# Kernel optimization log

Measured on AMD Instinct MI355X. Metric: run time of the kernel, lower is better.

The kernel has to match this reference:

```python
import jax, jax.numpy as jnp
import numpy as np

N = 50000        # links * batches
E = 1000000      # edges per frame
T = 10           # frame_num
H = 8            # graph_embedding_size


def setup_inputs() -> dict:
    key = jax.random.key(0)
    ks = jax.random.split(key, 20)
    w = lambda k, s: (jax.random.normal(k, s, jnp.float32) * 0.1)
    return {
        "x": jax.random.normal(ks[0], (N, T, 2), jnp.float32),
        "edge_index": jax.random.randint(ks[1], (2, T, E), 0, N),
        "edge_attr": jax.random.uniform(ks[2], (E, T, 1), jnp.float32),
        # mlp1: [1+H, 32, 32] + Lin(32,1)+Sigmoid
        "m1_w1": w(ks[3], (1 + H, 32)), "m1_b1": jnp.zeros((32,), jnp.float32),
        "m1_w2": w(ks[4], (32, 32)),     "m1_b2": jnp.zeros((32,), jnp.float32),
        "m1_w3": w(ks[5], (32, 1)),      "m1_b3": jnp.zeros((1,), jnp.float32),
        # mlp2: [1+1+H, 32, H]
        "m2_w1": w(ks[6], (2 + H, 32)),  "m2_b1": jnp.zeros((32,), jnp.float32),
        "m2_w2": w(ks[7], (32, H)),      "m2_b2": jnp.zeros((H,), jnp.float32),
        # h2o: [H, 16] + Lin(16,1)+Sigmoid
        "o_w1": w(ks[8], (H, 16)),       "o_b1": jnp.zeros((16,), jnp.float32),
        "o_w2": w(ks[9], (16, 1)),       "o_b2": jnp.zeros((1,), jnp.float32),
    }


def reference(x, edge_index, edge_attr,
              m1_w1, m1_b1, m1_w2, m1_b2, m1_w3, m1_b3,
              m2_w1, m2_b1, m2_w2, m2_b2,
              o_w1, o_b1, o_w2, o_b2):
    n_nodes = x.shape[0]
    hid = m2_b2.shape[0]
    AGG_MEAN, AGG_VAR = 0.0, 1.0  # undefined globals in source; identity norm

    def step(hidden, inputs):
        x_t, ei_t, ea_t = inputs                 # [N,2], [2,E], [E,1]
        xh = jnp.concatenate([x_t, hidden], 1)   # [N, 2+H]
        src, dst = ei_t[0], ei_t[1]              # PyG: x_j = x[src], agg at dst
        xj = xh[src]                             # [E, 2+H] gather
        feat = jnp.concatenate([xj[:, :1], xj[:, 2:]], 1)  # [E, 1+H]
        h = jax.nn.relu(feat @ m1_w1 + m1_b1)
        h = jax.nn.relu(h @ m1_w2 + m1_b2)
        msg = jax.nn.sigmoid(h @ m1_w3 + m1_b3) * ea_t      # [E,1]
        agg = jax.ops.segment_sum(msg, dst, num_segments=n_nodes)  # [N,1]
        norm = (agg - AGG_MEAN) / AGG_VAR
        upd_in = jnp.concatenate([xh[:, 1:], norm], 1)      # [N, 2+H]
        u = jax.nn.relu(upd_in @ m2_w1 + m2_b1)
        u = jax.nn.relu(u @ m2_w2 + m2_b2)
        hidden_new = jnp.tanh(u)                            # [N,H]
        o = jax.nn.relu(hidden_new @ o_w1 + o_b1)
        out = jax.nn.sigmoid(o @ o_w2 + o_b2)               # [N,1]
        return hidden_new, out

    x_seq = jnp.transpose(x, (1, 0, 2))            # [T,N,2]
    ei_seq = jnp.transpose(edge_index, (1, 0, 2))  # [T,2,E]
    ea_seq = jnp.transpose(edge_attr, (1, 0, 2))   # [T,E,1]
    h0 = jnp.zeros((n_nodes, hid), x.dtype)
    _, outs = jax.lax.scan(step, h0, (x_seq, ei_seq, ea_seq))
    return outs  # [T, N, 1]
```

## Files before the change

kernel.cpp:

```cpp
#include <hip/hip_runtime.h>

#define NN 50000
#define TT 10
#define EE 1000000

#define NB 391
#define BN 128
#define NBP 512
#define CAP 3072
#define CHUNK 2048
#define NCHUNK 489
#define KPT (CHUNK / 256)
#define SPILLCAP 8192

__device__ __forceinline__ float sigmoidf_(float v) { return 1.0f / (1.0f + __expf(-v)); }
__device__ __forceinline__ float reluf_(float v) { return v > 0.0f ? v : 0.0f; }

__device__ __forceinline__ float4 ld4_(const float* __restrict__ p) {
    return *reinterpret_cast<const float4*>(p);
}
__device__ __forceinline__ void fma_row8(float* acc, const float* __restrict__ w, float f) {
    float4 a = ld4_(w), b = ld4_(w + 4);
    acc[0] += f * a.x; acc[1] += f * a.y; acc[2] += f * a.z; acc[3] += f * a.w;
    acc[4] += f * b.x; acc[5] += f * b.y; acc[6] += f * b.z; acc[7] += f * b.w;
}

__device__ __forceinline__ float mlp1_eval_g(const float* feat,
                                             const float* __restrict__ w1,
                                             const float* __restrict__ b1,
                                             const float* __restrict__ w2,
                                             const float* __restrict__ b2,
                                             const float* __restrict__ w3,
                                             const float* __restrict__ b3) {
    float h1[32];
#pragma unroll
    for (int j = 0; j < 32; ++j) h1[j] = b1[j];
#pragma unroll
    for (int i = 0; i < 9; ++i) {
        float f = feat[i];
#pragma unroll
        for (int j = 0; j < 32; ++j) h1[j] += f * w1[i * 32 + j];
    }
#pragma unroll
    for (int j = 0; j < 32; ++j) h1[j] = reluf_(h1[j]);
    float h2[32];
#pragma unroll
    for (int j = 0; j < 32; ++j) h2[j] = b2[j];
#pragma unroll
    for (int i = 0; i < 32; ++i) {
        float f = h1[i];
#pragma unroll
        for (int j = 0; j < 32; ++j) h2[j] += f * w2[i * 32 + j];
    }
    float acc = b3[0];
#pragma unroll
    for (int j = 0; j < 32; ++j) acc += reluf_(h2[j]) * w3[j];
    return sigmoidf_(acc);
}

__global__ void pre_kernel(const float* __restrict__ x,
                           const float* __restrict__ w1, const float* __restrict__ b1,
                           const float* __restrict__ w2, const float* __restrict__ b2,
                           const float* __restrict__ w3, const float* __restrict__ b3,
                           float* __restrict__ hidden, float* __restrict__ msg_base,
                           float* __restrict__ agg,
                           float* __restrict__ x0T, float* __restrict__ x1T,
                           unsigned* __restrict__ gcnt, unsigned* __restrict__ spillCnt,
                           int sorted) {
    int g = blockIdx.x * blockDim.x + threadIdx.x;
    if (g < NB * TT) gcnt[g] = 0u;
    if (g == 0) spillCnt[0] = 0u;
    if (g >= NN) return;
    float x00;
    if (sorted) {
        const float2* xr = reinterpret_cast<const float2*>(x + (size_t)g * TT * 2);
        float x0v[TT], x1v[TT];
#pragma unroll
        for (int tt = 0; tt < TT; ++tt) { float2 p = xr[tt]; x0v[tt] = p.x; x1v[tt] = p.y; }
#pragma unroll
        for (int tt = 0; tt < TT; ++tt) { x0T[tt * NN + g] = x0v[tt]; x1T[tt * NN + g] = x1v[tt]; }
        x00 = x0v[0];
    } else {
        x00 = x[(size_t)g * TT * 2];
    }
    agg[g] = 0.0f;
    float feat[9];
    feat[0] = x00;
#pragma unroll
    for (int k = 0; k < 8; ++k) feat[1 + k] = 0.0f;
    msg_base[g] = mlp1_eval_g(feat, w1, b1, w2, b2, w3, b3);
#pragma unroll
    for (int k = 0; k < 8; ++k) hidden[g * 8 + k] = 0.0f;
}

__global__ __launch_bounds__(256) void reorder_kernel(const int* __restrict__ ei,
                                                      const float* __restrict__ ea,
                                                      unsigned* __restrict__ gcnt,
                                                      int4* __restrict__ regions,
                                                      int4* __restrict__ spill,
                                                      unsigned* __restrict__ spillCnt) {
    __shared__ int4 stg[CHUNK];
    __shared__ unsigned h4[4][NBP];
    __shared__ unsigned lbase[NBP], cur[NBP], gbase[NBP];
    __shared__ unsigned bscan[256];
    __shared__ unsigned cnt_s;
    const int t = blockIdx.x, c = blockIdx.y;
    const int tid = threadIdx.x, w = tid >> 6;

    for (int i = tid; i < 4 * NBP; i += 256) (&h4[0][0])[i] = 0u;
    __syncthreads();

    const int* srcp = ei + (size_t)t * EE;
    const int* dstp = ei + (size_t)(TT + t) * EE;
    int se[KPT], de[KPT];
    float ev[KPT];
#pragma unroll
    for (int k = 0; k < KPT; ++k) {
        int e = c * CHUNK + k * 256 + tid;
        if (e < EE) {
            se[k] = srcp[e];
            de[k] = dstp[e];
            ev[k] = ea[(size_t)e * TT + t];
            atomicAdd(&h4[w][(unsigned)de[k] >> 7], 1u);
        } else {
            de[k] = -1; se[k] = 0; ev[k] = 0.0f;
        }
    }
    __syncthreads();

    unsigned c0 = h4[0][2 * tid] + h4[1][2 * tid] + h4[2][2 * tid] + h4[3][2 * tid];
    unsigned c1 = h4[0][2 * tid + 1] + h4[1][2 * tid + 1] + h4[2][2 * tid + 1] + h4[3][2 * tid + 1];
    unsigned mys = c0 + c1;
    bscan[tid] = mys;
    __syncthreads();
    for (int off = 1; off < 256; off <<= 1) {
        unsigned vv = (tid >= off) ? bscan[tid - off] : 0u;
        __syncthreads();
        bscan[tid] += vv;
        __syncthreads();
    }
    unsigned excl = bscan[tid] - mys;
    lbase[2 * tid] = excl;           cur[2 * tid] = excl;
    lbase[2 * tid + 1] = excl + c0;  cur[2 * tid + 1] = excl + c0;
    if (tid == 255) cnt_s = bscan[255];
    {
        int b0 = 2 * tid, b1 = 2 * tid + 1;
        gbase[b0] = (b0 < NB) ? atomicAdd(&gcnt[t * NB + b0], c0) : 0u;
        gbase[b1] = (b1 < NB) ? atomicAdd(&gcnt[t * NB + b1], c1) : 0u;
    }
    __syncthreads();

#pragma unroll
    for (int k = 0; k < KPT; ++k) {
        if (de[k] >= 0) {
            unsigned b = (unsigned)de[k] >> 7;
            unsigned slot = atomicAdd(&cur[b], 1u);
            stg[slot] = make_int4(se[k], de[k], __float_as_int(ev[k]), 0);
        }
    }
    __syncthreads();

    const unsigned cnt = cnt_s;
    for (unsigned i = tid; i < cnt; i += 256) {
        int4 rec = stg[i];
        unsigned b = (unsigned)rec.y >> 7;
        unsigned g = gbase[b] + (i - lbase[b]);
        if (g < CAP) {
            regions[((size_t)(t * NB + b)) * CAP + g] = rec;
        } else {
            unsigned sp = atomicAdd(spillCnt, 1u);
            if (sp < SPILLCAP) spill[sp] = make_int4(rec.x, rec.y, rec.z, t);
        }
    }
}

__global__ __launch_bounds__(512) void edge_node_kernel(
        const float* __restrict__ x0T, const float* __restrict__ x1T,
        const int4* __restrict__ regions, const unsigned* __restrict__ gcnt,
        const int4* __restrict__ spill, const unsigned* __restrict__ spillCnt,
        const float* __restrict__ m1w1, const float* __restrict__ m1b1,
        const float* __restrict__ m1w2, const float* __restrict__ m1b2,
        const float* __restrict__ m1w3, const float* __restrict__ m1b3,
        const float* __restrict__ m2w1, const float* __restrict__ m2b1,
        const float* __restrict__ m2w2, const float* __restrict__ m2b2,
        const float* __restrict__ ow1, const float* __restrict__ ob1,
        const float* __restrict__ ow2, const float* __restrict__ ob2,
        float* __restrict__ hidden, float* __restrict__ msg_base,
        float* __restrict__ out, int t) {
    __shared__ float acc_s[BN];
    const int b = blockIdx.x, tid = threadIdx.x;
    if (tid < BN) acc_s[tid] = 0.0f;
    __syncthreads();

    {
        unsigned cnt = gcnt[t * NB + b];
        if (cnt > CAP) cnt = CAP;
        const int4* p = regions + ((size_t)(t * NB + b)) * CAP;
        for (unsigned i = tid; i < cnt; i += 512) {
            int4 rec = p[i];
            atomicAdd(&acc_s[rec.y & (BN - 1)], msg_base[rec.x] * __int_as_float(rec.z));
        }
        unsigned sp = spillCnt[0];
        for (unsigned j = tid; j < sp; j += 512) {
            int4 rec = spill[j];
            if (rec.w == t && ((unsigned)rec.y >> 7) == (unsigned)b)
                atomicAdd(&acc_s[rec.y & (BN - 1)], msg_base[rec.x] * __int_as_float(rec.z));
        }
    }
    __syncthreads();

    const int n = b * BN + (tid >> 2);
    const int q = tid & 3;
    if (n >= NN) return;

    const float a = acc_s[tid >> 2];
    const float x1 = x1T[t * NN + n];

    float2 hme = *reinterpret_cast<const float2*>(hidden + (size_t)n * 8 + q * 2);
    float hid[8];
    hid[0] = hme.x; hid[1] = hme.y;
    hid[2] = __shfl_xor(hid[0], 1); hid[3] = __shfl_xor(hid[1], 1);
    hid[4] = __shfl_xor(hid[0], 2); hid[5] = __shfl_xor(hid[1], 2);
    hid[6] = __shfl_xor(hid[2], 2); hid[7] = __shfl_xor(hid[3], 2);

    float acc[8];
    {
        float4 bA = ld4_(m2b1 + q * 8), bB = ld4_(m2b1 + q * 8 + 4);
        acc[0] = bA.x; acc[1] = bA.y; acc[2] = bA.z; acc[3] = bA.w;
        acc[4] = bB.x; acc[5] = bB.y; acc[6] = bB.z; acc[7] = bB.w;
    }
    fma_row8(acc, m2w1 + q * 8, x1);
#pragma unroll
    for (int g = 0; g < 4; ++g) {
        int rq = (q ^ g) * 2;
        fma_row8(acc, m2w1 + (size_t)(1 + rq) * 32 + q * 8, hid[g * 2 + 0]);
        fma_row8(acc, m2w1 + (size_t)(2 + rq) * 32 + q * 8, hid[g * 2 + 1]);
    }
    fma_row8(acc, m2w1 + (size_t)9 * 32 + q * 8, a);
    float u1[8];
#pragma unroll
    for (int jj = 0; jj < 8; ++jj) u1[jj] = reluf_(acc[jj]);

    float pk[8];
#pragma unroll
    for (int k = 0; k < 8; ++k) pk[k] = 0.0f;
#pragma unroll
    for (int jj = 0; jj < 8; ++jj)
        fma_row8(pk, m2w2 + (size_t)(q * 8 + jj) * 8, u1[jj]);
#pragma unroll
    for (int k = 0; k < 8; ++k) {
        pk[k] += __shfl_xor(pk[k], 1);
        pk[k] += __shfl_xor(pk[k], 2);
    }
    float hn[8];
    {
        float4 b2A = ld4_(m2b2), b2B = ld4_(m2b2 + 4);
        hn[0] = tanhf(reluf_(pk[0] + b2A.x));
        hn[1] = tanhf(reluf_(pk[1] + b2A.y));
        hn[2] = tanhf(reluf_(pk[2] + b2A.z));
        hn[3] = tanhf(reluf_(pk[3] + b2A.w));
        hn[4] = tanhf(reluf_(pk[4] + b2B.x));
        hn[5] = tanhf(reluf_(pk[5] + b2B.y));
        hn[6] = tanhf(reluf_(pk[6] + b2B.z));
        hn[7] = tanhf(reluf_(pk[7] + b2B.w));
    }
    if (q == 0) {
        *reinterpret_cast<float4*>(hidden + (size_t)n * 8)     = make_float4(hn[0], hn[1], hn[2], hn[3]);
        *reinterpret_cast<float4*>(hidden + (size_t)n * 8 + 4) = make_float4(hn[4], hn[5], hn[6], hn[7]);
    }

    float o1v[4];
    {
        float4 ob = ld4_(ob1 + q * 4);
        o1v[0] = ob.x; o1v[1] = ob.y; o1v[2] = ob.z; o1v[3] = ob.w;
    }
#pragma unroll
    for (int k = 0; k < 8; ++k) {
        float4 wv = ld4_(ow1 + k * 16 + q * 4);
        o1v[0] += hn[k] * wv.x; o1v[1] += hn[k] * wv.y;
        o1v[2] += hn[k] * wv.z; o1v[3] += hn[k] * wv.w;
    }
    {
        float4 w2v = ld4_(ow2 + q * 4);
        float oop = reluf_(o1v[0]) * w2v.x + reluf_(o1v[1]) * w2v.y +
                    reluf_(o1v[2]) * w2v.z + reluf_(o1v[3]) * w2v.w;
        oop += __shfl_xor(oop, 1);
        oop += __shfl_xor(oop, 2);
        if (q == 0) out[t * NN + n] = sigmoidf_(oop + ob2[0]);
    }

    if (t < TT - 1) {
        float feat0 = x0T[(t + 1) * NN + n];
        float h1[8];
        {
            float4 bA = ld4_(m1b1 + q * 8), bB = ld4_(m1b1 + q * 8 + 4);
            h1[0] = bA.x; h1[1] = bA.y; h1[2] = bA.z; h1[3] = bA.w;
            h1[4] = bB.x; h1[5] = bB.y; h1[6] = bB.z; h1[7] = bB.w;
        }
        fma_row8(h1, m1w1 + q * 8, feat0);
#pragma unroll
        for (int k = 0; k < 8; ++k)
            fma_row8(h1, m1w1 + (size_t)(1 + k) * 32 + q * 8, hn[k]);
#pragma unroll
        for (int jj = 0; jj < 8; ++jj) h1[jj] = reluf_(h1[jj]);

        float h1x[32];
#pragma unroll
        for (int jj = 0; jj < 8; ++jj) h1x[jj] = h1[jj];
#pragma unroll
        for (int jj = 0; jj < 8; ++jj) h1x[8 + jj]  = __shfl_xor(h1x[jj], 1);
#pragma unroll
        for (int jj = 0; jj < 8; ++jj) h1x[16 + jj] = __shfl_xor(h1x[jj], 2);
#pragma unroll
        for (int jj = 0; jj < 8; ++jj) h1x[24 + jj] = __shfl_xor(h1x[8 + jj], 2);

        float acc8[8];
        {
            float4 bA = ld4_(m1b2 + q * 8), bB = ld4_(m1b2 + q * 8 + 4);
            acc8[0] = bA.x; acc8[1] = bA.y; acc8[2] = bA.z; acc8[3] = bA.w;
            acc8[4] = bB.x; acc8[5] = bB.y; acc8[6] = bB.z; acc8[7] = bB.w;
        }
#pragma unroll
        for (int g = 0; g < 4; ++g) {
            int rb = (q ^ g) * 8;
#pragma unroll
            for (int jj = 0; jj < 8; ++jj)
                fma_row8(acc8, m1w2 + (size_t)(rb + jj) * 32 + q * 8, h1x[g * 8 + jj]);
        }
        float s3;
        {
            float4 w3a = ld4_(m1w3 + q * 8), w3b = ld4_(m1w3 + q * 8 + 4);
            s3 = reluf_(acc8[0]) * w3a.x + reluf_(acc8[1]) * w3a.y +
                 reluf_(acc8[2]) * w3a.z + reluf_(acc8[3]) * w3a.w +
                 reluf_(acc8[4]) * w3b.x + reluf_(acc8[5]) * w3b.y +
                 reluf_(acc8[6]) * w3b.z + reluf_(acc8[7]) * w3b.w;
        }
        s3 += __shfl_xor(s3, 1);
        s3 += __shfl_xor(s3, 2);
        if (q == 0) msg_base[n] = sigmoidf_(s3 + m1b3[0]);
    }
}

__global__ void edge_kernel(const int* __restrict__ ei, const float* __restrict__ ea,
                            const float* __restrict__ msg_base, float* __restrict__ agg,
                            int t) {
    int g = blockIdx.x * blockDim.x + threadIdx.x;
    int e0 = g * 2;
    if (e0 >= EE) return;
    const int2 s = *reinterpret_cast<const int2*>(ei + (size_t)t * EE + e0);
    const int2 d = *reinterpret_cast<const int2*>(ei + (size_t)(TT + t) * EE + e0);
    atomicAdd(&agg[d.x], msg_base[s.x] * ea[(size_t)e0 * TT + t]);
    atomicAdd(&agg[d.y], msg_base[s.y] * ea[(size_t)(e0 + 1) * TT + t]);
}

__global__ __launch_bounds__(256) void node4_legacy_kernel(
        const float* __restrict__ x,
        const float* __restrict__ m1w1, const float* __restrict__ m1b1,
        const float* __restrict__ m1w2, const float* __restrict__ m1b2,
        const float* __restrict__ m1w3, const float* __restrict__ m1b3,
        const float* __restrict__ m2w1, const float* __restrict__ m2b1,
        const float* __restrict__ m2w2, const float* __restrict__ m2b2,
        const float* __restrict__ ow1, const float* __restrict__ ob1,
        const float* __restrict__ ow2, const float* __restrict__ ob2,
        float* __restrict__ hidden, float* __restrict__ msg_base,
        float* __restrict__ agg, float* __restrict__ out, int t) {
    const int gid = blockIdx.x * 256 + threadIdx.x;
    const int n = gid >> 2;
    const int q = gid & 3;
    if (n >= NN) return;
    const float a = agg[n];
    const float x1 = x[(size_t)n * TT * 2 + t * 2 + 1];
    float2 hme = *reinterpret_cast<const float2*>(hidden + (size_t)n * 8 + q * 2);
    float hid[8];
    hid[0] = hme.x; hid[1] = hme.y;
    hid[2] = __shfl_xor(hid[0], 1); hid[3] = __shfl_xor(hid[1], 1);
    hid[4] = __shfl_xor(hid[0], 2); hid[5] = __shfl_xor(hid[1], 2);
    hid[6] = __shfl_xor(hid[2], 2); hid[7] = __shfl_xor(hid[3], 2);
    float acc[8];
    {
        float4 bA = ld4_(m2b1 + q * 8), bB = ld4_(m2b1 + q * 8 + 4);
        acc[0] = bA.x; acc[1] = bA.y; acc[2] = bA.z; acc[3] = bA.w;
        acc[4] = bB.x; acc[5] = bB.y; acc[6] = bB.z; acc[7] = bB.w;
    }
    fma_row8(acc, m2w1 + q * 8, x1);
#pragma unroll
    for (int g = 0; g < 4; ++g) {
        int rq = (q ^ g) * 2;
        fma_row8(acc, m2w1 + (size_t)(1 + rq) * 32 + q * 8, hid[g * 2 + 0]);
        fma_row8(acc, m2w1 + (size_t)(2 + rq) * 32 + q * 8, hid[g * 2 + 1]);
    }
    fma_row8(acc, m2w1 + (size_t)9 * 32 + q * 8, a);
    float u1[8];
#pragma unroll
    for (int jj = 0; jj < 8; ++jj) u1[jj] = reluf_(acc[jj]);
    float pk[8];
#pragma unroll
    for (int k = 0; k < 8; ++k) pk[k] = 0.0f;
#pragma unroll
    for (int jj = 0; jj < 8; ++jj)
        fma_row8(pk, m2w2 + (size_t)(q * 8 + jj) * 8, u1[jj]);
#pragma unroll
    for (int k = 0; k < 8; ++k) {
        pk[k] += __shfl_xor(pk[k], 1);
        pk[k] += __shfl_xor(pk[k], 2);
    }
    float hn[8];
    {
        float4 b2A = ld4_(m2b2), b2B = ld4_(m2b2 + 4);
        hn[0] = tanhf(reluf_(pk[0] + b2A.x));
        hn[1] = tanhf(reluf_(pk[1] + b2A.y));
        hn[2] = tanhf(reluf_(pk[2] + b2A.z));
        hn[3] = tanhf(reluf_(pk[3] + b2A.w));
        hn[4] = tanhf(reluf_(pk[4] + b2B.x));
        hn[5] = tanhf(reluf_(pk[5] + b2B.y));
        hn[6] = tanhf(reluf_(pk[6] + b2B.z));
        hn[7] = tanhf(reluf_(pk[7] + b2B.w));
    }
    if (q == 0) {
        *reinterpret_cast<float4*>(hidden + (size_t)n * 8)     = make_float4(hn[0], hn[1], hn[2], hn[3]);
        *reinterpret_cast<float4*>(hidden + (size_t)n * 8 + 4) = make_float4(hn[4], hn[5], hn[6], hn[7]);
    }
    float o1v[4];
    {
        float4 ob = ld4_(ob1 + q * 4);
        o1v[0] = ob.x; o1v[1] = ob.y; o1v[2] = ob.z; o1v[3] = ob.w;
    }
#pragma unroll
    for (int k = 0; k < 8; ++k) {
        float4 wv = ld4_(ow1 + k * 16 + q * 4);
        o1v[0] += hn[k] * wv.x; o1v[1] += hn[k] * wv.y;
        o1v[2] += hn[k] * wv.z; o1v[3] += hn[k] * wv.w;
    }
    {
        float4 w2v = ld4_(ow2 + q * 4);
        float oop = reluf_(o1v[0]) * w2v.x + reluf_(o1v[1]) * w2v.y +
                    reluf_(o1v[2]) * w2v.z + reluf_(o1v[3]) * w2v.w;
        oop += __shfl_xor(oop, 1);
        oop += __shfl_xor(oop, 2);
        if (q == 0) out[t * NN + n] = sigmoidf_(oop + ob2[0]);
    }
    if (t < TT - 1) {
        float feat0 = x[(size_t)n * TT * 2 + (t + 1) * 2];
        float h1[8];
        {
            float4 bA = ld4_(m1b1 + q * 8), bB = ld4_(m1b1 + q * 8 + 4);
            h1[0] = bA.x; h1[1] = bA.y; h1[2] = bA.z; h1[3] = bA.w;
            h1[4] = bB.x; h1[5] = bB.y; h1[6] = bB.z; h1[7] = bB.w;
        }
        fma_row8(h1, m1w1 + q * 8, feat0);
#pragma unroll
        for (int k = 0; k < 8; ++k)
            fma_row8(h1, m1w1 + (size_t)(1 + k) * 32 + q * 8, hn[k]);
#pragma unroll
        for (int jj = 0; jj < 8; ++jj) h1[jj] = reluf_(h1[jj]);
        float h1x[32];
#pragma unroll
        for (int jj = 0; jj < 8; ++jj) h1x[jj] = h1[jj];
#pragma unroll
        for (int jj = 0; jj < 8; ++jj) h1x[8 + jj]  = __shfl_xor(h1x[jj], 1);
#pragma unroll
        for (int jj = 0; jj < 8; ++jj) h1x[16 + jj] = __shfl_xor(h1x[jj], 2);
#pragma unroll
        for (int jj = 0; jj < 8; ++jj) h1x[24 + jj] = __shfl_xor(h1x[8 + jj], 2);
        float acc8[8];
        {
            float4 bA = ld4_(m1b2 + q * 8), bB = ld4_(m1b2 + q * 8 + 4);
            acc8[0] = bA.x; acc8[1] = bA.y; acc8[2] = bA.z; acc8[3] = bA.w;
            acc8[4] = bB.x; acc8[5] = bB.y; acc8[6] = bB.z; acc8[7] = bB.w;
        }
#pragma unroll
        for (int g = 0; g < 4; ++g) {
            int rb = (q ^ g) * 8;
#pragma unroll
            for (int jj = 0; jj < 8; ++jj)
                fma_row8(acc8, m1w2 + (size_t)(rb + jj) * 32 + q * 8, h1x[g * 8 + jj]);
        }
        float s3;
        {
            float4 w3a = ld4_(m1w3 + q * 8), w3b = ld4_(m1w3 + q * 8 + 4);
            s3 = reluf_(acc8[0]) * w3a.x + reluf_(acc8[1]) * w3a.y +
                 reluf_(acc8[2]) * w3a.z + reluf_(acc8[3]) * w3a.w +
                 reluf_(acc8[4]) * w3b.x + reluf_(acc8[5]) * w3b.y +
                 reluf_(acc8[6]) * w3b.z + reluf_(acc8[7]) * w3b.w;
        }
        s3 += __shfl_xor(s3, 1);
        s3 += __shfl_xor(s3, 2);
        if (q == 0) {
            msg_base[n] = sigmoidf_(s3 + m1b3[0]);
            agg[n] = 0.0f;
        }
    }
}

extern "C" void kernel_launch(void* const* d_in, const int* in_sizes, int n_in,
                              void* d_out, int out_size, void* d_ws, size_t ws_size,
                              hipStream_t stream) {
    (void)in_sizes; (void)n_in; (void)out_size;
    const float* x    = (const float*)d_in[0];
    const int*   ei   = (const int*)d_in[1];
    const float* ea   = (const float*)d_in[2];
    const float* m1w1 = (const float*)d_in[3];
    const float* m1b1 = (const float*)d_in[4];
    const float* m1w2 = (const float*)d_in[5];
    const float* m1b2 = (const float*)d_in[6];
    const float* m1w3 = (const float*)d_in[7];
    const float* m1b3 = (const float*)d_in[8];
    const float* m2w1 = (const float*)d_in[9];
    const float* m2b1 = (const float*)d_in[10];
    const float* m2w2 = (const float*)d_in[11];
    const float* m2b2 = (const float*)d_in[12];
    const float* ow1  = (const float*)d_in[13];
    const float* ob1  = (const float*)d_in[14];
    const float* ow2  = (const float*)d_in[15];
    const float* ob2  = (const float*)d_in[16];
    float* out = (float*)d_out;

    char* wp = (char*)d_ws;
    float* hidden   = (float*)wp; wp += (size_t)NN * 8 * 4;
    float* msg_base = (float*)wp; wp += (size_t)NN * 4;
    float* agg      = (float*)wp; wp += (size_t)NN * 4;
    float* x0T      = (float*)wp; wp += (size_t)NN * TT * 4;
    float* x1T      = (float*)wp; wp += (size_t)NN * TT * 4;
    int4*  regions  = (int4*)wp;  wp += (size_t)NB * TT * CAP * 16;
    int4*  spill    = (int4*)wp;  wp += (size_t)SPILLCAP * 16;
    unsigned* gcnt    = (unsigned*)wp; wp += (size_t)NB * TT * 4;
    unsigned* spillCnt = (unsigned*)wp; wp += 64;
    size_t need = (size_t)(wp - (char*)d_ws);

    int sorted = (ws_size >= need) ? 1 : 0;

    dim3 blk(256);
    int nodeBlocks = (NN + 255) / 256;
    int edgeBlocksLegacy = (EE / 2 + 255) / 256;
    int node4BlocksLegacy = (NN * 4 + 255) / 256;

    pre_kernel<<<nodeBlocks, blk, 0, stream>>>(x, m1w1, m1b1, m1w2, m1b2, m1w3, m1b3,
                                               hidden, msg_base, agg, x0T, x1T,
                                               gcnt, spillCnt, sorted);
    if (sorted) {
        reorder_kernel<<<dim3(TT, NCHUNK), blk, 0, stream>>>(ei, ea, gcnt, regions,
                                                             spill, spillCnt);
        for (int t = 0; t < TT; ++t) {
            edge_node_kernel<<<NB, dim3(512), 0, stream>>>(
                x0T, x1T, regions, gcnt, spill, spillCnt,
                m1w1, m1b1, m1w2, m1b2, m1w3, m1b3,
                m2w1, m2b1, m2w2, m2b2,
                ow1, ob1, ow2, ob2,
                hidden, msg_base, out, t);
        }
    } else {
        for (int t = 0; t < TT; ++t) {
            edge_kernel<<<edgeBlocksLegacy, blk, 0, stream>>>(ei, ea, msg_base, agg, t);
            node4_legacy_kernel<<<node4BlocksLegacy, blk, 0, stream>>>(
                x, m1w1, m1b1, m1w2, m1b2, m1w3, m1b3,
                m2w1, m2b1, m2w2, m2b2,
                ow1, ob1, ow2, ob2,
                hidden, msg_base, agg, out, t);
        }
    }
}
```

Baseline: 593.9 us.

## Transpose edge attrs, pack region records, stage weights in LDS, double-buffer messages

The pre kernel now transposes edge_attr into a frame-major buffer so the reorder kernel reads it coalesced instead of with a stride of 10 floats. Region records shrink from int4 to int2 by packing the source index and the local destination into one word, which halves region write and read traffic. The edge_node kernel stages all MLP weights in shared memory rather than reading them from global memory. Message values are double-buffered (msgA/msgB) to fix a read/write race on msg_base across blocks. The cost is an extra 40MB transpose pass and a larger workspace requirement, which may make the sorted path fall back if the workspace is too small.

```diff
diff --git a/kernel.cpp b/kernel.cpp
--- a/kernel.cpp
+++ b/kernel.cpp
@@ -13,19 +13,36 @@
 #define KPT (CHUNK / 256)
 #define SPILLCAP 8192
 
+#define OFF_M2W1 0
+#define OFF_M2B1 320
+#define OFF_M2W2 352
+#define OFF_M2B2 608
+#define OFF_OW1  616
+#define OFF_OB1  744
+#define OFF_OW2  760
+#define OFF_M1W1 776
+#define OFF_M1B1 1064
+#define OFF_M1W2 1096
+#define OFF_M1B2 2120
+#define OFF_M1W3 2152
+#define OFF_OB2  2184
+#define OFF_M1B3 2185
+#define WTOT     2188
+
 __device__ __forceinline__ float sigmoidf_(float v) { return 1.0f / (1.0f + __expf(-v)); }
 __device__ __forceinline__ float reluf_(float v) { return v > 0.0f ? v : 0.0f; }
 
 __device__ __forceinline__ float4 ld4_(const float* __restrict__ p) {
     return *reinterpret_cast<const float4*>(p);
 }
-__device__ __forceinline__ void fma_row8(float* acc, const float* __restrict__ w, float f) {
-    float4 a = ld4_(w), b = ld4_(w + 4);
+__device__ __forceinline__ void fma_row8(float* acc, const float* w, float f) {
+    float4 a = *reinterpret_cast<const float4*>(w);
+    float4 b = *reinterpret_cast<const float4*>(w + 4);
     acc[0] += f * a.x; acc[1] += f * a.y; acc[2] += f * a.z; acc[3] += f * a.w;
     acc[4] += f * b.x; acc[5] += f * b.y; acc[6] += f * b.z; acc[7] += f * b.w;
 }
 
-__device__ __forceinline__ float mlp1_eval_g(const float* feat,
+__device__ __forceinline__ float mlp1_frame0(float x00,
                                              const float* __restrict__ w1,
                                              const float* __restrict__ b1,
                                              const float* __restrict__ w2,
@@ -34,15 +51,7 @@
                                              const float* __restrict__ b3) {
     float h1[32];
 #pragma unroll
-    for (int j = 0; j < 32; ++j) h1[j] = b1[j];
-#pragma unroll
-    for (int i = 0; i < 9; ++i) {
-        float f = feat[i];
-#pragma unroll
-        for (int j = 0; j < 32; ++j) h1[j] += f * w1[i * 32 + j];
-    }
-#pragma unroll
-    for (int j = 0; j < 32; ++j) h1[j] = reluf_(h1[j]);
+    for (int j = 0; j < 32; ++j) h1[j] = reluf_(b1[j] + x00 * w1[j]);
     float h2[32];
 #pragma unroll
     for (int j = 0; j < 32; ++j) h2[j] = b2[j];
@@ -59,17 +68,29 @@
 }
 
 __global__ void pre_kernel(const float* __restrict__ x,
+                           const float* __restrict__ ea,
                            const float* __restrict__ w1, const float* __restrict__ b1,
                            const float* __restrict__ w2, const float* __restrict__ b2,
                            const float* __restrict__ w3, const float* __restrict__ b3,
-                           float* __restrict__ hidden, float* __restrict__ msg_base,
+                           float* __restrict__ hidden, float* __restrict__ msgA,
                            float* __restrict__ agg,
                            float* __restrict__ x0T, float* __restrict__ x1T,
+                           float* __restrict__ eaT,
                            unsigned* __restrict__ gcnt, unsigned* __restrict__ spillCnt,
                            int sorted) {
     int g = blockIdx.x * blockDim.x + threadIdx.x;
-    if (g < NB * TT) gcnt[g] = 0u;
-    if (g == 0) spillCnt[0] = 0u;
+    if (sorted) {
+        if (g < EE) {
+            const float2* row = reinterpret_cast<const float2*>(ea + (size_t)g * TT);
+            float v[TT];
+#pragma unroll
+            for (int c = 0; c < 5; ++c) { float2 p = row[c]; v[2 * c] = p.x; v[2 * c + 1] = p.y; }
+#pragma unroll
+            for (int tt = 0; tt < TT; ++tt) eaT[(size_t)tt * EE + g] = v[tt];
+        }
+        if (g < NB * TT) gcnt[g] = 0u;
+        if (g == 0) spillCnt[0] = 0u;
+    }
     if (g >= NN) return;
     float x00;
     if (sorted) {
@@ -84,19 +105,15 @@
         x00 = x[(size_t)g * TT * 2];
     }
     agg[g] = 0.0f;
-    float feat[9];
-    feat[0] = x00;
-#pragma unroll
-    for (int k = 0; k < 8; ++k) feat[1 + k] = 0.0f;
-    msg_base[g] = mlp1_eval_g(feat, w1, b1, w2, b2, w3, b3);
+    msgA[g] = mlp1_frame0(x00, w1, b1, w2, b2, w3, b3);
 #pragma unroll
     for (int k = 0; k < 8; ++k) hidden[g * 8 + k] = 0.0f;
 }
 
 __global__ __launch_bounds__(256) void reorder_kernel(const int* __restrict__ ei,
-                                                      const float* __restrict__ ea,
+                                                      const float* __restrict__ eaT,
                                                       unsigned* __restrict__ gcnt,
-                                                      int4* __restrict__ regions,
+                                                      int2* __restrict__ regions,
                                                       int4* __restrict__ spill,
                                                       unsigned* __restrict__ spillCnt) {
     __shared__ int4 stg[CHUNK];
@@ -120,7 +137,7 @@
         if (e < EE) {
             se[k] = srcp[e];
             de[k] = dstp[e];
-            ev[k] = ea[(size_t)e * TT + t];
+            ev[k] = eaT[(size_t)t * EE + e];
             atomicAdd(&h4[w][(unsigned)de[k] >> 7], 1u);
         } else {
             de[k] = -1; se[k] = 0; ev[k] = 0.0f;
@@ -166,7 +183,8 @@
         unsigned b = (unsigned)rec.y >> 7;
         unsigned g = gbase[b] + (i - lbase[b]);
         if (g < CAP) {
-            regions[((size_t)(t * NB + b)) * CAP + g] = rec;
+            unsigned u = (unsigned)rec.x | (((unsigned)rec.y & 127u) << 17);
+            regions[((size_t)(t * NB + b)) * CAP + g] = make_int2((int)u, rec.z);
         } else {
             unsigned sp = atomicAdd(spillCnt, 1u);
             if (sp < SPILLCAP) spill[sp] = make_int4(rec.x, rec.y, rec.z, t);
@@ -176,7 +194,7 @@
 
 __global__ __launch_bounds__(512) void edge_node_kernel(
         const float* __restrict__ x0T, const float* __restrict__ x1T,
-        const int4* __restrict__ regions, const unsigned* __restrict__ gcnt,
+        const int2* __restrict__ regions, const unsigned* __restrict__ gcnt,
         const int4* __restrict__ spill, const unsigned* __restrict__ spillCnt,
         const float* __restrict__ m1w1, const float* __restrict__ m1b1,
         const float* __restrict__ m1w2, const float* __restrict__ m1b2,
@@ -185,26 +203,45 @@
         const float* __restrict__ m2w2, const float* __restrict__ m2b2,
         const float* __restrict__ ow1, const float* __restrict__ ob1,
         const float* __restrict__ ow2, const float* __restrict__ ob2,
-        float* __restrict__ hidden, float* __restrict__ msg_base,
-        float* __restrict__ out, int t) {
+        float* __restrict__ hidden, const float* __restrict__ msgIn,
+        float* __restrict__ msgOut, float* __restrict__ out, int t) {
+    __shared__ __align__(16) float wsh[WTOT];
     __shared__ float acc_s[BN];
     const int b = blockIdx.x, tid = threadIdx.x;
+
+    for (int i = tid; i < 320; i += 512) wsh[OFF_M2W1 + i] = m2w1[i];
+    for (int i = tid; i < 256; i += 512) wsh[OFF_M2W2 + i] = m2w2[i];
+    for (int i = tid; i < 288; i += 512) wsh[OFF_M1W1 + i] = m1w1[i];
+    for (int i = tid; i < 1024; i += 512) wsh[OFF_M1W2 + i] = m1w2[i];
+    if (tid < 32) {
+        wsh[OFF_M2B1 + tid] = m2b1[tid];
+        wsh[OFF_M1B1 + tid] = m1b1[tid];
+        wsh[OFF_M1B2 + tid] = m1b2[tid];
+        wsh[OFF_M1W3 + tid] = m1w3[tid];
+    }
+    if (tid >= 32 && tid < 40) wsh[OFF_M2B2 + tid - 32] = m2b2[tid - 32];
+    if (tid >= 64 && tid < 192) wsh[OFF_OW1 + tid - 64] = ow1[tid - 64];
+    if (tid >= 192 && tid < 208) wsh[OFF_OB1 + tid - 192] = ob1[tid - 192];
+    if (tid >= 208 && tid < 224) wsh[OFF_OW2 + tid - 208] = ow2[tid - 208];
+    if (tid == 224) wsh[OFF_OB2] = ob2[0];
+    if (tid == 225) wsh[OFF_M1B3] = m1b3[0];
     if (tid < BN) acc_s[tid] = 0.0f;
     __syncthreads();
 
     {
         unsigned cnt = gcnt[t * NB + b];
         if (cnt > CAP) cnt = CAP;
-        const int4* p = regions + ((size_t)(t * NB + b)) * CAP;
+        const int2* p = regions + ((size_t)(t * NB + b)) * CAP;
         for (unsigned i = tid; i < cnt; i += 512) {
-            int4 rec = p[i];
-            atomicAdd(&acc_s[rec.y & (BN - 1)], msg_base[rec.x] * __int_as_float(rec.z));
+            int2 rec = p[i];
+            unsigned u = (unsigned)rec.x;
+            atomicAdd(&acc_s[u >> 17], msgIn[u & 0x1FFFFu] * __int_as_float(rec.y));
         }
         unsigned sp = spillCnt[0];
         for (unsigned j = tid; j < sp; j += 512) {
             int4 rec = spill[j];
             if (rec.w == t && ((unsigned)rec.y >> 7) == (unsigned)b)
-                atomicAdd(&acc_s[rec.y & (BN - 1)], msg_base[rec.x] * __int_as_float(rec.z));
+                atomicAdd(&acc_s[rec.y & (BN - 1)], msgIn[rec.x] * __int_as_float(rec.z));
         }
     }
     __syncthreads();
@@ -225,18 +262,18 @@
 
     float acc[8];
     {
-        float4 bA = ld4_(m2b1 + q * 8), bB = ld4_(m2b1 + q * 8 + 4);
+        float4 bA = ld4_(&wsh[OFF_M2B1 + q * 8]), bB = ld4_(&wsh[OFF_M2B1 + q * 8 + 4]);
         acc[0] = bA.x; acc[1] = bA.y; acc[2] = bA.z; acc[3] = bA.w;
         acc[4] = bB.x; acc[5] = bB.y; acc[6] = bB.z; acc[7] = bB.w;
     }
-    fma_row8(acc, m2w1 + q * 8, x1);
+    fma_row8(acc, &wsh[OFF_M2W1 + q * 8], x1);
 #pragma unroll
     for (int g = 0; g < 4; ++g) {
         int rq = (q ^ g) * 2;
-        fma_row8(acc, m2w1 + (size_t)(1 + rq) * 32 + q * 8, hid[g * 2 + 0]);
-        fma_row8(acc, m2w1 + (size_t)(2 + rq) * 32 + q * 8, hid[g * 2 + 1]);
-    }
-    fma_row8(acc, m2w1 + (size_t)9 * 32 + q * 8, a);
+        fma_row8(acc, &wsh[OFF_M2W1 + (1 + rq) * 32 + q * 8], hid[g * 2 + 0]);
+        fma_row8(acc, &wsh[OFF_M2W1 + (2 + rq) * 32 + q * 8], hid[g * 2 + 1]);
+    }
+    fma_row8(acc, &wsh[OFF_M2W1 + 9 * 32 + q * 8], a);
     float u1[8];
 #pragma unroll
     for (int jj = 0; jj < 8; ++jj) u1[jj] = reluf_(acc[jj]);
@@ -246,7 +283,7 @@
     for (int k = 0; k < 8; ++k) pk[k] = 0.0f;
 #pragma unroll
     for (int jj = 0; jj < 8; ++jj)
-        fma_row8(pk, m2w2 + (size_t)(q * 8 + jj) * 8, u1[jj]);
+        fma_row8(pk, &wsh[OFF_M2W2 + (q * 8 + jj) * 8], u1[jj]);
 #pragma unroll
     for (int k = 0; k < 8; ++k) {
         pk[k] += __shfl_xor(pk[k], 1);
@@ -254,7 +291,7 @@
     }
     float hn[8];
     {
-        float4 b2A = ld4_(m2b2), b2B = ld4_(m2b2 + 4);
+        float4 b2A = ld4_(&wsh[OFF_M2B2]), b2B = ld4_(&wsh[OFF_M2B2 + 4]);
         hn[0] = tanhf(reluf_(pk[0] + b2A.x));
         hn[1] = tanhf(reluf_(pk[1] + b2A.y));
         hn[2] = tanhf(reluf_(pk[2] + b2A.z));
@@ -271,36 +308,36 @@
 
     float o1v[4];
     {
-        float4 ob = ld4_(ob1 + q * 4);
+        float4 ob = ld4_(&wsh[OFF_OB1 + q * 4]);
         o1v[0] = ob.x; o1v[1] = ob.y; o1v[2] = ob.z; o1v[3] = ob.w;
     }
 #pragma unroll
     for (int k = 0; k < 8; ++k) {
-        float4 wv = ld4_(ow1 + k * 16 + q * 4);
+        float4 wv = ld4_(&wsh[OFF_OW1 + k * 16 + q * 4]);
         o1v[0] += hn[k] * wv.x; o1v[1] += hn[k] * wv.y;
         o1v[2] += hn[k] * wv.z; o1v[3] += hn[k] * wv.w;
     }
     {
-        float4 w2v = ld4_(ow2 + q * 4);
+        float4 w2v = ld4_(&wsh[OFF_OW2 + q * 4]);
         float oop = reluf_(o1v[0]) * w2v.x + reluf_(o1v[1]) * w2v.y +
                     reluf_(o1v[2]) * w2v.z + reluf_(o1v[3]) * w2v.w;
         oop += __shfl_xor(oop, 1);
         oop += __shfl_xor(oop, 2);
-        if (q == 0) out[t * NN + n] = sigmoidf_(oop + ob2[0]);
+        if (q == 0) out[t * NN + n] = sigmoidf_(oop + wsh[OFF_OB2]);
     }
 
     if (t < TT - 1) {
         float feat0 = x0T[(t + 1) * NN + n];
         float h1[8];
         {
-            float4 bA = ld4_(m1b1 + q * 8), bB = ld4_(m1b1 + q * 8 + 4);
+            float4 bA = ld4_(&wsh[OFF_M1B1 + q * 8]), bB = ld4_(&wsh[OFF_M1B1 + q * 8 + 4]);
             h1[0] = bA.x; h1[1] = bA.y; h1[2] = bA.z; h1[3] = bA.w;
             h1[4] = bB.x; h1[5] = bB.y; h1[6] = bB.z; h1[7] = bB.w;
         }
-        fma_row8(h1, m1w1 + q * 8, feat0);
+        fma_row8(h1, &wsh[OFF_M1W1 + q * 8], feat0);
 #pragma unroll
         for (int k = 0; k < 8; ++k)
-            fma_row8(h1, m1w1 + (size_t)(1 + k) * 32 + q * 8, hn[k]);
+            fma_row8(h1, &wsh[OFF_M1W1 + (1 + k) * 32 + q * 8], hn[k]);
 #pragma unroll
         for (int jj = 0; jj < 8; ++jj) h1[jj] = reluf_(h1[jj]);
 
@@ -316,7 +353,7 @@
 
         float acc8[8];
         {
-            float4 bA = ld4_(m1b2 + q * 8), bB = ld4_(m1b2 + q * 8 + 4);
+            float4 bA = ld4_(&wsh[OFF_M1B2 + q * 8]), bB = ld4_(&wsh[OFF_M1B2 + q * 8 + 4]);
             acc8[0] = bA.x; acc8[1] = bA.y; acc8[2] = bA.z; acc8[3] = bA.w;
             acc8[4] = bB.x; acc8[5] = bB.y; acc8[6] = bB.z; acc8[7] = bB.w;
         }
@@ -325,11 +362,11 @@
             int rb = (q ^ g) * 8;
 #pragma unroll
             for (int jj = 0; jj < 8; ++jj)
-                fma_row8(acc8, m1w2 + (size_t)(rb + jj) * 32 + q * 8, h1x[g * 8 + jj]);
+                fma_row8(acc8, &wsh[OFF_M1W2 + (rb + jj) * 32 + q * 8], h1x[g * 8 + jj]);
         }
         float s3;
         {
-            float4 w3a = ld4_(m1w3 + q * 8), w3b = ld4_(m1w3 + q * 8 + 4);
+            float4 w3a = ld4_(&wsh[OFF_M1W3 + q * 8]), w3b = ld4_(&wsh[OFF_M1W3 + q * 8 + 4]);
             s3 = reluf_(acc8[0]) * w3a.x + reluf_(acc8[1]) * w3a.y +
                  reluf_(acc8[2]) * w3a.z + reluf_(acc8[3]) * w3a.w +
                  reluf_(acc8[4]) * w3b.x + reluf_(acc8[5]) * w3b.y +
@@ -337,7 +374,7 @@
         }
         s3 += __shfl_xor(s3, 1);
         s3 += __shfl_xor(s3, 2);
-        if (q == 0) msg_base[n] = sigmoidf_(s3 + m1b3[0]);
+        if (q == 0) msgOut[n] = sigmoidf_(s3 + wsh[OFF_M1B3]);
     }
 }
 
@@ -517,11 +554,13 @@
 
     char* wp = (char*)d_ws;
     float* hidden   = (float*)wp; wp += (size_t)NN * 8 * 4;
-    float* msg_base = (float*)wp; wp += (size_t)NN * 4;
+    float* msgA     = (float*)wp; wp += (size_t)NN * 4;
+    float* msgB     = (float*)wp; wp += (size_t)NN * 4;
     float* agg      = (float*)wp; wp += (size_t)NN * 4;
     float* x0T      = (float*)wp; wp += (size_t)NN * TT * 4;
     float* x1T      = (float*)wp; wp += (size_t)NN * TT * 4;
-    int4*  regions  = (int4*)wp;  wp += (size_t)NB * TT * CAP * 16;
+    float* eaT      = (float*)wp; wp += (size_t)TT * EE * 4;
+    int2*  regions  = (int2*)wp;  wp += (size_t)NB * TT * CAP * 8;
     int4*  spill    = (int4*)wp;  wp += (size_t)SPILLCAP * 16;
     unsigned* gcnt    = (unsigned*)wp; wp += (size_t)NB * TT * 4;
     unsigned* spillCnt = (unsigned*)wp; wp += 64;
@@ -531,31 +570,34 @@
 
     dim3 blk(256);
     int nodeBlocks = (NN + 255) / 256;
+    int preBlocks = sorted ? (EE + 255) / 256 : nodeBlocks;
     int edgeBlocksLegacy = (EE / 2 + 255) / 256;
     int node4BlocksLegacy = (NN * 4 + 255) / 256;
 
-    pre_kernel<<<nodeBlocks, blk, 0, stream>>>(x, m1w1, m1b1, m1w2, m1b2, m1w3, m1b3,
-                                               hidden, msg_base, agg, x0T, x1T,
-                                               gcnt, spillCnt, sorted);
+    pre_kernel<<<preBlocks, blk, 0, stream>>>(x, ea, m1w1, m1b1, m1w2, m1b2, m1w3, m1b3,
+                                              hidden, msgA, agg, x0T, x1T, eaT,
+                                              gcnt, spillCnt, sorted);
     if (sorted) {
-        reorder_kernel<<<dim3(TT, NCHUNK), blk, 0, stream>>>(ei, ea, gcnt, regions,
+        reorder_kernel<<<dim3(TT, NCHUNK), blk, 0, stream>>>(ei, eaT, gcnt, regions,
                                                              spill, spillCnt);
         for (int t = 0; t < TT; ++t) {
+            const float* msgIn = (t & 1) ? msgB : msgA;
+            float* msgOut = (t & 1) ? msgA : msgB;
             edge_node_kernel<<<NB, dim3(512), 0, stream>>>(
                 x0T, x1T, regions, gcnt, spill, spillCnt,
                 m1w1, m1b1, m1w2, m1b2, m1w3, m1b3,
                 m2w1, m2b1, m2w2, m2b2,
                 ow1, ob1, ow2, ob2,
-                hidden, msg_base, out, t);
+                hidden, msgIn, msgOut, out, t);
         }
     } else {
         for (int t = 0; t < TT; ++t) {
-            edge_kernel<<<edgeBlocksLegacy, blk, 0, stream>>>(ei, ea, msg_base, agg, t);
+            edge_kernel<<<edgeBlocksLegacy, blk, 0, stream>>>(ei, ea, msgA, agg, t);
             node4_legacy_kernel<<<node4BlocksLegacy, blk, 0, stream>>>(
                 x, m1w1, m1b1, m1w2, m1b2, m1w3, m1b3,
                 m2w1, m2b1, m2w2, m2b2,
                 ow1, ob1, ow2, ob2,
-                hidden, msg_base, agg, out, t);
-        }
-    }
-}
+                hidden, msgA, agg, out, t);
+        }
+    }
+}
```

New measurement: 485.7 us. 1.22x faster.
